# Optimization experiments

Measured on AMD Instinct MI355X. Metric: run time of the kernel, lower is better.

## Reference

```python
import jax, jax.numpy as jnp
import numpy as np

D = 1024
H = 16
HD = D // H
FF = 4 * D
EPS = 1e-6


def layernorm(x, g, b):
    mu = jnp.mean(x, axis=-1, keepdims=True)
    var = jnp.mean((x - mu) ** 2, axis=-1, keepdims=True)
    return (x - mu) * jax.lax.rsqrt(var + EPS) * g + b


def setup_inputs() -> dict:
    key = jax.random.key(0)
    ks = jax.random.split(key, 12)
    s = 0.02
    return {
        "x": jax.random.normal(ks[0], (8, 1024, D), dtype=jnp.float32),
        "qkv_w": jax.random.normal(ks[1], (3 * D, D), dtype=jnp.float32) * s,
        "qkv_b": jnp.zeros((3 * D,), dtype=jnp.float32),
        "proj_w": jax.random.normal(ks[2], (D, D), dtype=jnp.float32) * s,
        "proj_b": jnp.zeros((D,), dtype=jnp.float32),
        "fc1_w": jax.random.normal(ks[3], (FF, D), dtype=jnp.float32) * s,
        "fc1_b": jnp.zeros((FF,), dtype=jnp.float32),
        "fc2_w": jax.random.normal(ks[4], (D, FF), dtype=jnp.float32) * s,
        "fc2_b": jnp.zeros((D,), dtype=jnp.float32),
        "ln1_g": jnp.ones((D,), dtype=jnp.float32),
        "ln1_b": jnp.zeros((D,), dtype=jnp.float32),
        "ln2_g": jnp.ones((D,), dtype=jnp.float32),
        "ln2_b": jnp.zeros((D,), dtype=jnp.float32),
    }


def reference(x, qkv_w, qkv_b, proj_w, proj_b, fc1_w, fc1_b, fc2_w, fc2_b,
              ln1_g, ln1_b, ln2_g, ln2_b):
    B, S, _ = x.shape
    # attention branch
    h = layernorm(x, ln1_g, ln1_b)
    qkv = h @ qkv_w.T + qkv_b                      # [B,S,3D]
    qkv = qkv.reshape(B, S, 3, H, HD)
    q, k, v = qkv[:, :, 0], qkv[:, :, 1], qkv[:, :, 2]  # [B,S,H,HD]
    scores = jnp.einsum('bshd,bthd->bhst', q, k) * (HD ** -0.5)
    attn = jax.nn.softmax(scores, axis=-1)
    ctx = jnp.einsum('bhst,bthd->bshd', attn, v).reshape(B, S, D)
    x = x + ctx @ proj_w.T + proj_b
    # mlp branch
    h = layernorm(x, ln2_g, ln2_b)
    h = jax.nn.gelu(h @ fc1_w.T + fc1_b, approximate=False)
    x = x + h @ fc2_w.T + fc2_b
    return x
```

## Files before the change

kernel.cpp:

```cpp
#include <hip/hip_runtime.h>
#include <stdint.h>

typedef unsigned short u16;
typedef __attribute__((ext_vector_type(8))) short bf16x8;
typedef __attribute__((ext_vector_type(4))) short bf16x4;
typedef __attribute__((ext_vector_type(4))) float f32x4;

__device__ __forceinline__ u16 f2bf(float f) {
    union { float f; uint32_t u; } v; v.f = f;
    uint32_t r = (v.u + 0x7FFFu + ((v.u >> 16) & 1u)) >> 16;
    return (u16)r;
}

__device__ __forceinline__ void g2l16(const u16* g, u16* l) {
    __builtin_amdgcn_global_load_lds(
        (const __attribute__((address_space(1))) uint32_t*)g,
        (__attribute__((address_space(3))) uint32_t*)l, 16, 0, 0);
}

__global__ __launch_bounds__(256) void cvt_kernel(const float* __restrict__ in,
                                                  u16* __restrict__ out, int n4) {
    int i = blockIdx.x * 256 + threadIdx.x;
    if (i < n4) {
        float4 v = ((const float4*)in)[i];
        uint2 o;
        o.x = (uint32_t)f2bf(v.x) | ((uint32_t)f2bf(v.y) << 16);
        o.y = (uint32_t)f2bf(v.z) | ((uint32_t)f2bf(v.w) << 16);
        ((uint2*)out)[i] = o;
    }
}

__global__ __launch_bounds__(256) void ln_kernel(const float* __restrict__ x,
                                                 const float* __restrict__ g,
                                                 const float* __restrict__ beta,
                                                 u16* __restrict__ out) {
    int row = blockIdx.x;
    int tid = threadIdx.x;
    const float4 v = ((const float4*)(x + (size_t)row * 1024))[tid];
    float s  = v.x + v.y + v.z + v.w;
    float sq = v.x*v.x + v.y*v.y + v.z*v.z + v.w*v.w;
    #pragma unroll
    for (int off = 32; off; off >>= 1) {
        s  += __shfl_xor(s,  off, 64);
        sq += __shfl_xor(sq, off, 64);
    }
    __shared__ float rs[4], rq[4];
    int w = tid >> 6;
    if ((tid & 63) == 0) { rs[w] = s; rq[w] = sq; }
    __syncthreads();
    s  = rs[0] + rs[1] + rs[2] + rs[3];
    sq = rq[0] + rq[1] + rq[2] + rq[3];
    float mu   = s * (1.0f / 1024.0f);
    float var  = sq * (1.0f / 1024.0f) - mu * mu;
    float rstd = rsqrtf(var + 1e-6f);
    float4 gv = ((const float4*)g)[tid];
    float4 bv = ((const float4*)beta)[tid];
    uint2 o;
    o.x = (uint32_t)f2bf((v.x - mu) * rstd * gv.x + bv.x) |
          ((uint32_t)f2bf((v.y - mu) * rstd * gv.y + bv.y) << 16);
    o.y = (uint32_t)f2bf((v.z - mu) * rstd * gv.z + bv.z) |
          ((uint32_t)f2bf((v.w - mu) * rstd * gv.w + bv.w) << 16);
    ((uint2*)(out + (size_t)row * 1024))[tid] = o;
}

template<int ACT, int RES, int OUTBF>
__global__ __launch_bounds__(256) void gemm_kernel(
    const u16* __restrict__ A, const u16* __restrict__ W,
    const float* __restrict__ bias, const float* __restrict__ res,
    void* __restrict__ Cout, int M, int N, int K)
{
    __shared__ u16 sA[128 * 64];
    __shared__ u16 sB[128 * 64];
    int tid = threadIdx.x;
    int lane = tid & 63, wid = tid >> 6;
    int wm = wid >> 1, wn = wid & 1;
    int ntiles = N >> 7;
    int m0 = (blockIdx.x / ntiles) << 7;
    int n0 = (blockIdx.x % ntiles) << 7;
    int q = lane & 15, g = lane >> 4;

    f32x4 acc[4][4];
    #pragma unroll
    for (int i = 0; i < 4; i++)
        #pragma unroll
        for (int j = 0; j < 4; j++)
            acc[i][j] = (f32x4){0.f, 0.f, 0.f, 0.f};

    for (int k0 = 0; k0 < K; k0 += 64) {
        __syncthreads();
        #pragma unroll
        for (int c = 0; c < 4; c++) {
            int flat = ((c * 4 + wid) * 64 + lane) * 8;
            int r = flat >> 6, cc = flat & 63;
            g2l16(A + (size_t)(m0 + r) * K + k0 + cc, sA + (c * 4 + wid) * 512);
            g2l16(W + (size_t)(n0 + r) * K + k0 + cc, sB + (c * 4 + wid) * 512);
        }
        __syncthreads();
        #pragma unroll
        for (int ks = 0; ks < 2; ks++) {
            bf16x8 af[4], bfr[4];
            #pragma unroll
            for (int i = 0; i < 4; i++) {
                af[i]  = *(const bf16x8*)(sA + (wm * 64 + i * 16 + q) * 64 + ks * 32 + g * 8);
                bfr[i] = *(const bf16x8*)(sB + (wn * 64 + i * 16 + q) * 64 + ks * 32 + g * 8);
            }
            #pragma unroll
            for (int i = 0; i < 4; i++)
                #pragma unroll
                for (int j = 0; j < 4; j++)
                    acc[i][j] = __builtin_amdgcn_mfma_f32_16x16x32_bf16(af[i], bfr[j], acc[i][j], 0, 0, 0);
        }
    }

    #pragma unroll
    for (int i = 0; i < 4; i++) {
        #pragma unroll
        for (int j = 0; j < 4; j++) {
            int col = n0 + wn * 64 + j * 16 + q;
            float bz = bias[col];
            #pragma unroll
            for (int r = 0; r < 4; r++) {
                int row = m0 + wm * 64 + i * 16 + g * 4 + r;
                float v = acc[i][j][r] + bz;
                if (ACT == 1) v = 0.5f * v * (1.0f + erff(v * 0.70710678118654752f));
                if (RES) v += res[(size_t)row * N + col];
                if (OUTBF) ((u16*)Cout)[(size_t)row * N + col] = f2bf(v);
                else       ((float*)Cout)[(size_t)row * N + col] = v;
            }
        }
    }
}

__global__ __launch_bounds__(256) void attn_kernel(const u16* __restrict__ qkv,
                                                   u16* __restrict__ ctx) {
    int bid = blockIdx.x;
    int qt = bid & 15;
    int h  = (bid >> 4) & 15;
    int b  = bid >> 8;
    int tid = threadIdx.x, lane = tid & 63, w = tid >> 6;
    int q = lane & 15, g = lane >> 4;

    __shared__ u16 sQ[64 * 72];
    __shared__ u16 sK[32 * 72];
    __shared__ u16 sVT[64 * 36];

    const size_t tokBase = ((size_t)b * 1024) * 3072 + (size_t)h * 64;
    const float SC = 0.125f * 1.44269504088896f;

    #pragma unroll
    for (int p = 0; p < 2; p++) {
        int flat = (p * 256 + tid) * 8;
        int r = flat >> 6, c = flat & 63;
        uint4 v = *(const uint4*)(qkv + tokBase + (size_t)(qt * 64 + r) * 3072 + c);
        *(uint4*)(sQ + r * 72 + c) = v;
    }
    __syncthreads();
    bf16x8 qf0 = *(const bf16x8*)(sQ + (w * 16 + q) * 72 + g * 8);
    bf16x8 qf1 = *(const bf16x8*)(sQ + (w * 16 + q) * 72 + 32 + g * 8);

    float m_run = -1e30f, l_run = 0.0f;
    f32x4 o[4];
    #pragma unroll
    for (int n = 0; n < 4; n++) o[n] = (f32x4){0.f, 0.f, 0.f, 0.f};

    int kr = tid >> 3, kc = (tid & 7) * 8;
    int kperm = ((kr >> 2) & 3) * 8 + (kr >> 4) * 4 + (kr & 3);

    for (int kt = 0; kt < 32; kt++) {
        __syncthreads();
        {
            uint4 v = *(const uint4*)(qkv + tokBase + (size_t)(kt * 32 + kperm) * 3072 + 1024 + kc);
            *(uint4*)(sK + kr * 72 + kc) = v;
        }
        #pragma unroll
        for (int p = 0; p < 2; p++) {
            int flat = (p * 256 + tid) * 4;
            int key = flat >> 6, cc = flat & 63;
            ushort4 vv = *(const ushort4*)(qkv + tokBase + (size_t)(kt * 32 + key) * 3072 + 2048 + cc);
            sVT[(cc + 0) * 36 + key] = vv.x;
            sVT[(cc + 1) * 36 + key] = vv.y;
            sVT[(cc + 2) * 36 + key] = vv.z;
            sVT[(cc + 3) * 36 + key] = vv.w;
        }
        __syncthreads();

        f32x4 s0 = (f32x4){0.f, 0.f, 0.f, 0.f}, s1 = s0;
        {
            bf16x8 k00 = *(const bf16x8*)(sK + (q) * 72 + g * 8);
            bf16x8 k01 = *(const bf16x8*)(sK + (q) * 72 + 32 + g * 8);
            s0 = __builtin_amdgcn_mfma_f32_16x16x32_bf16(k00, qf0, s0, 0, 0, 0);
            s0 = __builtin_amdgcn_mfma_f32_16x16x32_bf16(k01, qf1, s0, 0, 0, 0);
            bf16x8 k10 = *(const bf16x8*)(sK + (16 + q) * 72 + g * 8);
            bf16x8 k11 = *(const bf16x8*)(sK + (16 + q) * 72 + 32 + g * 8);
            s1 = __builtin_amdgcn_mfma_f32_16x16x32_bf16(k10, qf0, s1, 0, 0, 0);
            s1 = __builtin_amdgcn_mfma_f32_16x16x32_bf16(k11, qf1, s1, 0, 0, 0);
        }
        float ps[8];
        #pragma unroll
        for (int r = 0; r < 4; r++) { ps[r] = s0[r] * SC; ps[4 + r] = s1[r] * SC; }
        float tm = ps[0];
        #pragma unroll
        for (int i = 1; i < 8; i++) tm = fmaxf(tm, ps[i]);
        tm = fmaxf(tm, __shfl_xor(tm, 16, 64));
        tm = fmaxf(tm, __shfl_xor(tm, 32, 64));

        if (!__all(tm - m_run <= 8.0f)) {
            float nm = fmaxf(m_run, tm);
            float f = exp2f(m_run - nm);
            float fr[4];
            #pragma unroll
            for (int r = 0; r < 4; r++) fr[r] = __shfl(f, g * 4 + r, 64);
            #pragma unroll
            for (int n = 0; n < 4; n++)
                #pragma unroll
                for (int r = 0; r < 4; r++) o[n][r] *= fr[r];
            l_run *= f;
            m_run = nm;
        }

        float ts = 0.0f;
        #pragma unroll
        for (int i = 0; i < 8; i++) { ps[i] = exp2f(ps[i] - m_run); ts += ps[i]; }
        ts += __shfl_xor(ts, 16, 64);
        ts += __shfl_xor(ts, 32, 64);
        l_run += ts;

        bf16x8 pf;
        #pragma unroll
        for (int j = 0; j < 8; j++) pf[j] = (short)f2bf(ps[j]);

        #pragma unroll
        for (int n = 0; n < 4; n++) {
            bf16x4 vlo = *(const bf16x4*)(sVT + (n * 16 + q) * 36 + g * 8);
            bf16x4 vhi = *(const bf16x4*)(sVT + (n * 16 + q) * 36 + g * 8 + 4);
            bf16x8 vf;
            #pragma unroll
            for (int j = 0; j < 4; j++) { vf[j] = vlo[j]; vf[4 + j] = vhi[j]; }
            o[n] = __builtin_amdgcn_mfma_f32_16x16x32_bf16(pf, vf, o[n], 0, 0, 0);
        }
    }

    float inv = 1.0f / l_run;
    float ir[4];
    #pragma unroll
    for (int r = 0; r < 4; r++) ir[r] = __shfl(inv, g * 4 + r, 64);
    size_t outBase = ((size_t)b * 1024 + qt * 64 + w * 16) * 1024 + (size_t)h * 64;
    #pragma unroll
    for (int n = 0; n < 4; n++)
        #pragma unroll
        for (int r = 0; r < 4; r++)
            ctx[outBase + (size_t)(g * 4 + r) * 1024 + n * 16 + q] = f2bf(o[n][r] * ir[r]);
}

extern "C" void kernel_launch(void* const* d_in, const int* in_sizes, int n_in,
                              void* d_out, int out_size, void* d_ws, size_t ws_size,
                              hipStream_t stream) {
    const float* x      = (const float*)d_in[0];
    const float* qkv_w  = (const float*)d_in[1];
    const float* qkv_b  = (const float*)d_in[2];
    const float* proj_w = (const float*)d_in[3];
    const float* proj_b = (const float*)d_in[4];
    const float* fc1_w  = (const float*)d_in[5];
    const float* fc1_b  = (const float*)d_in[6];
    const float* fc2_w  = (const float*)d_in[7];
    const float* fc2_b  = (const float*)d_in[8];
    const float* ln1_g  = (const float*)d_in[9];
    const float* ln1_b  = (const float*)d_in[10];
    const float* ln2_g  = (const float*)d_in[11];
    const float* ln2_b  = (const float*)d_in[12];
    float* out = (float*)d_out;

    char* ws = (char*)d_ws;
    u16* wq = (u16*)(ws);
    u16* wp = (u16*)(ws + 6291456);
    u16* w1 = (u16*)(ws + 8388608);
    u16* w2 = (u16*)(ws + 16777216);
    char* pool = ws + 25165824;
    u16* hbuf = (u16*)(pool);
    u16* qkvb = (u16*)(pool + 16777216);
    u16* ctxb = (u16*)(pool);
    u16* h2b  = (u16*)(pool + 16777216);
    u16* a1b  = (u16*)(pool + 33554432);

    cvt_kernel<<<3072, 256, 0, stream>>>(qkv_w, wq, 786432);
    cvt_kernel<<<1024, 256, 0, stream>>>(proj_w, wp, 262144);
    cvt_kernel<<<4096, 256, 0, stream>>>(fc1_w, w1, 1048576);
    cvt_kernel<<<4096, 256, 0, stream>>>(fc2_w, w2, 1048576);

    ln_kernel<<<8192, 256, 0, stream>>>(x, ln1_g, ln1_b, hbuf);
    gemm_kernel<0,0,1><<<64 * 24, 256, 0, stream>>>(hbuf, wq, qkv_b, nullptr, qkvb, 8192, 3072, 1024);
    attn_kernel<<<2048, 256, 0, stream>>>(qkvb, ctxb);
    gemm_kernel<0,1,0><<<64 * 8, 256, 0, stream>>>(ctxb, wp, proj_b, x, out, 8192, 1024, 1024);
    ln_kernel<<<8192, 256, 0, stream>>>(out, ln2_g, ln2_b, h2b);
    gemm_kernel<1,0,1><<<64 * 32, 256, 0, stream>>>(h2b, w1, fc1_b, nullptr, a1b, 8192, 4096, 1024);
    gemm_kernel<0,1,0><<<64 * 8, 256, 0, stream>>>(a1b, w2, fc2_b, out, out, 8192, 1024, 4096);
}
```

Measured before the change: 591.1 us.

## Replace GEMM with larger-tile double-buffered swizzled kernel and tanh GELU

Swaps the 128x128 single-buffered GEMM for a 512-thread kernel with 128x256 or 256x256 tiles. It double-buffers LDS so the next K-tile's global-to-LDS loads overlap the MFMAs on the current one. It XOR-swizzles the LDS layout to avoid bank conflicts and remaps block IDs so neighbouring tiles spread across XCDs for better L2 reuse. The erf GELU becomes a tanh approximation built on exp2, which trades some accuracy against the exact reference for fewer epilogue instructions. The larger tiles raise LDS and register pressure and allow only about one or two workgroups per CU.

```diff
diff --git a/kernel.cpp b/kernel.cpp
--- a/kernel.cpp
+++ b/kernel.cpp
@@ -16,6 +16,15 @@
     __builtin_amdgcn_global_load_lds(
         (const __attribute__((address_space(1))) uint32_t*)g,
         (__attribute__((address_space(3))) uint32_t*)l, 16, 0, 0);
+}
+
+__device__ __forceinline__ float gelu_f(float x) {
+    float x2 = x * x;
+    float u = x * (0.7978845608028654f + 0.035677408136300125f * x2);
+    float t = exp2f(-2.8853900817779268f * fabsf(u));
+    float th = (1.0f - t) / (1.0f + t);
+    th = (u < 0.0f) ? -th : th;
+    return 0.5f * x * (1.0f + th);
 }
 
 __global__ __launch_bounds__(256) void cvt_kernel(const float* __restrict__ in,
@@ -63,66 +72,96 @@
     ((uint2*)(out + (size_t)row * 1024))[tid] = o;
 }
 
-template<int ACT, int RES, int OUTBF>
-__global__ __launch_bounds__(256) void gemm_kernel(
+template<int M_REP, int ACT, int RES, int OUTBF>
+__global__ __launch_bounds__(512, 2) void gemm2_kernel(
     const u16* __restrict__ A, const u16* __restrict__ W,
     const float* __restrict__ bias, const float* __restrict__ res,
     void* __restrict__ Cout, int M, int N, int K)
 {
-    __shared__ u16 sA[128 * 64];
-    __shared__ u16 sB[128 * 64];
+    const int BM = M_REP * 32;
+    __shared__ u16 sA[2 * BM * 64];
+    __shared__ u16 sB[2 * 256 * 64];
+
     int tid = threadIdx.x;
     int lane = tid & 63, wid = tid >> 6;
-    int wm = wid >> 1, wn = wid & 1;
-    int ntiles = N >> 7;
-    int m0 = (blockIdx.x / ntiles) << 7;
-    int n0 = (blockIdx.x % ntiles) << 7;
+    int wm = wid >> 2, wn = wid & 3;
     int q = lane & 15, g = lane >> 4;
 
-    f32x4 acc[4][4];
-    #pragma unroll
-    for (int i = 0; i < 4; i++)
-        #pragma unroll
-        for (int j = 0; j < 4; j++)
-            acc[i][j] = (f32x4){0.f, 0.f, 0.f, 0.f};
-
-    for (int k0 = 0; k0 < K; k0 += 64) {
-        __syncthreads();
-        #pragma unroll
-        for (int c = 0; c < 4; c++) {
-            int flat = ((c * 4 + wid) * 64 + lane) * 8;
-            int r = flat >> 6, cc = flat & 63;
-            g2l16(A + (size_t)(m0 + r) * K + k0 + cc, sA + (c * 4 + wid) * 512);
-            g2l16(W + (size_t)(n0 + r) * K + k0 + cc, sB + (c * 4 + wid) * 512);
-        }
-        __syncthreads();
+    int MT = M / BM;
+    int nwg = gridDim.x;
+    int chunk = nwg >> 3;
+    int bid = blockIdx.x;
+    int wg = (bid & 7) * chunk + (bid >> 3);
+    int mt = wg % MT, nt = wg / MT;
+    int m0 = mt * BM, n0 = nt * 256;
+
+    const int NT = K >> 6;
+
+    f32x4 acc[M_REP][4] = {};
+
+    auto STAGE = [&](int buf, int k0) {
+        #pragma unroll
+        for (int l = 0; l < BM / 64; l++) {
+            int idx = l * 512 + tid;
+            int row = idx >> 3;
+            int col = ((idx & 7) * 8) ^ ((row & 7) << 3);
+            g2l16(A + (size_t)(m0 + row) * K + k0 + col,
+                  sA + buf * (BM * 64) + (l * 512 + wid * 64) * 8);
+        }
+        #pragma unroll
+        for (int l = 0; l < 4; l++) {
+            int idx = l * 512 + tid;
+            int row = idx >> 3;
+            int col = ((idx & 7) * 8) ^ ((row & 7) << 3);
+            g2l16(W + (size_t)(n0 + row) * K + k0 + col,
+                  sB + buf * (256 * 64) + (l * 512 + wid * 64) * 8);
+        }
+    };
+
+    STAGE(0, 0);
+    __syncthreads();
+
+    int buf = 0;
+    for (int t = 0; t < NT; t++) {
+        if (t + 1 < NT) STAGE(buf ^ 1, (t + 1) << 6);
+        const u16* bA = sA + buf * (BM * 64);
+        const u16* bB = sB + buf * (256 * 64);
         #pragma unroll
         for (int ks = 0; ks < 2; ks++) {
-            bf16x8 af[4], bfr[4];
-            #pragma unroll
-            for (int i = 0; i < 4; i++) {
-                af[i]  = *(const bf16x8*)(sA + (wm * 64 + i * 16 + q) * 64 + ks * 32 + g * 8);
-                bfr[i] = *(const bf16x8*)(sB + (wn * 64 + i * 16 + q) * 64 + ks * 32 + g * 8);
+            bf16x8 af[M_REP], bfr[4];
+            #pragma unroll
+            for (int i = 0; i < M_REP; i++) {
+                int rowL = wm * (BM / 2) + i * 16 + q;
+                int colE = (ks * 32 + g * 8) ^ ((rowL & 7) << 3);
+                af[i] = *(const bf16x8*)(bA + rowL * 64 + colE);
             }
             #pragma unroll
-            for (int i = 0; i < 4; i++)
+            for (int j = 0; j < 4; j++) {
+                int rowL = wn * 64 + j * 16 + q;
+                int colE = (ks * 32 + g * 8) ^ ((rowL & 7) << 3);
+                bfr[j] = *(const bf16x8*)(bB + rowL * 64 + colE);
+            }
+            #pragma unroll
+            for (int i = 0; i < M_REP; i++)
                 #pragma unroll
                 for (int j = 0; j < 4; j++)
                     acc[i][j] = __builtin_amdgcn_mfma_f32_16x16x32_bf16(af[i], bfr[j], acc[i][j], 0, 0, 0);
         }
-    }
-
-    #pragma unroll
-    for (int i = 0; i < 4; i++) {
+        __syncthreads();
+        buf ^= 1;
+    }
+
+    #pragma unroll
+    for (int i = 0; i < M_REP; i++) {
         #pragma unroll
         for (int j = 0; j < 4; j++) {
             int col = n0 + wn * 64 + j * 16 + q;
             float bz = bias[col];
             #pragma unroll
             for (int r = 0; r < 4; r++) {
-                int row = m0 + wm * 64 + i * 16 + g * 4 + r;
+                int row = m0 + wm * (BM / 2) + i * 16 + g * 4 + r;
                 float v = acc[i][j][r] + bz;
-                if (ACT == 1) v = 0.5f * v * (1.0f + erff(v * 0.70710678118654752f));
+                if (ACT == 1) v = gelu_f(v);
                 if (RES) v += res[(size_t)row * N + col];
                 if (OUTBF) ((u16*)Cout)[(size_t)row * N + col] = f2bf(v);
                 else       ((float*)Cout)[(size_t)row * N + col] = v;
@@ -288,10 +327,10 @@
     cvt_kernel<<<4096, 256, 0, stream>>>(fc2_w, w2, 1048576);
 
     ln_kernel<<<8192, 256, 0, stream>>>(x, ln1_g, ln1_b, hbuf);
-    gemm_kernel<0,0,1><<<64 * 24, 256, 0, stream>>>(hbuf, wq, qkv_b, nullptr, qkvb, 8192, 3072, 1024);
+    gemm2_kernel<4,0,0,1><<<768, 512, 0, stream>>>(hbuf, wq, qkv_b, nullptr, qkvb, 8192, 3072, 1024);
     attn_kernel<<<2048, 256, 0, stream>>>(qkvb, ctxb);
-    gemm_kernel<0,1,0><<<64 * 8, 256, 0, stream>>>(ctxb, wp, proj_b, x, out, 8192, 1024, 1024);
+    gemm2_kernel<4,0,1,0><<<256, 512, 0, stream>>>(ctxb, wp, proj_b, x, out, 8192, 1024, 1024);
     ln_kernel<<<8192, 256, 0, stream>>>(out, ln2_g, ln2_b, h2b);
-    gemm_kernel<1,0,1><<<64 * 32, 256, 0, stream>>>(h2b, w1, fc1_b, nullptr, a1b, 8192, 4096, 1024);
-    gemm_kernel<0,1,0><<<64 * 8, 256, 0, stream>>>(a1b, w2, fc2_b, out, out, 8192, 1024, 4096);
-}
+    gemm2_kernel<8,1,0,1><<<512, 512, 0, stream>>>(h2b, w1, fc1_b, nullptr, a1b, 8192, 4096, 1024);
+    gemm2_kernel<4,0,1,0><<<256, 512, 0, stream>>>(a1b, w2, fc2_b, out, out, 8192, 1024, 4096);
+}
```

Measured after the change: 563.2 us. 4.7% less time.
